# Kernel tuning notes

Hardware: AMD Instinct MI355X
Metric: run time of the kernel (lower is better)

## Reference

```python
import jax, jax.numpy as jnp
import numpy as np

E, IN, H1, H2, H3, A, B = 20, 512, 1024, 512, 256, 32, 4096


def setup_inputs() -> dict:
    key = jax.random.key(0)
    ks = jax.random.split(key, 10)

    def w(k, shape, fan_in):
        return jax.random.normal(k, shape, dtype=jnp.float32) / np.sqrt(fan_in)

    return {
        "obs": jax.random.normal(ks[0], (B, IN), dtype=jnp.float32),
        # stacked expert MLP params [E, ...]
        "eW1": w(ks[1], (E, IN, H1), IN), "eb1": jnp.zeros((E, H1), jnp.float32),
        "eW2": w(ks[2], (E, H1, H2), H1), "eb2": jnp.zeros((E, H2), jnp.float32),
        "eW3": w(ks[3], (E, H2, H3), H2), "eb3": jnp.zeros((E, H3), jnp.float32),
        "eW4": w(ks[4], (E, H3, A), H3), "eb4": jnp.zeros((E, A), jnp.float32),
        # gate MLP params
        "gW1": w(ks[5], (IN, H1), IN), "gb1": jnp.zeros((H1,), jnp.float32),
        "gW2": w(ks[6], (H1, H2), H1), "gb2": jnp.zeros((H2,), jnp.float32),
        "gW3": w(ks[7], (H2, H3), H2), "gb3": jnp.zeros((H3,), jnp.float32),
        "gW4": w(ks[8], (H3, E), H3), "gb4": jnp.zeros((E,), jnp.float32),
    }


def _experts(obs, eW1, eb1, eW2, eb2, eW3, eb3, eW4, eb4):
    # batched over experts: [B, E, h]
    h = jax.nn.elu(jnp.einsum('bi,eih->beh', obs, eW1) + eb1[None])
    h = jax.nn.elu(jnp.einsum('beh,ehk->bek', h, eW2) + eb2[None])
    h = jax.nn.elu(jnp.einsum('bek,ekm->bem', h, eW3) + eb3[None])
    return jnp.einsum('bem,ema->bea', h, eW4) + eb4[None]  # [B, E, A]


def _gate(obs, gW1, gb1, gW2, gb2, gW3, gb3, gW4, gb4):
    h = jax.nn.elu(obs @ gW1 + gb1)
    h = jax.nn.elu(h @ gW2 + gb2)
    h = jax.nn.elu(h @ gW3 + gb3)
    return jax.nn.softmax(h @ gW4 + gb4, axis=-1)  # [B, E]


def reference(obs, eW1, eb1, eW2, eb2, eW3, eb3, eW4, eb4,
              gW1, gb1, gW2, gb2, gW3, gb3, gW4, gb4):
    weights = _gate(obs, gW1, gb1, gW2, gb2, gW3, gb3, gW4, gb4)       # [B, E]
    actions = _experts(obs, eW1, eb1, eW2, eb2, eW3, eb3, eW4, eb4)    # [B, E, A]
    # bmm(weights[:,None,:], actions).squeeze(1)
    return jnp.einsum('be,bea->ba', weights, actions)                   # [B, A]
```

## Files before the change

kernel.cpp:

```cpp
#include <hip/hip_runtime.h>

#define B_SZ 4096
#define E_EXP 20
#define NE 21

typedef unsigned short u16;
typedef __bf16 bf16x8 __attribute__((ext_vector_type(8)));
typedef u16 u16x8 __attribute__((ext_vector_type(8)));
typedef u16 u16x4 __attribute__((ext_vector_type(4)));
typedef float floatx4 __attribute__((ext_vector_type(4)));

static __device__ __forceinline__ u16 f2bf(float f) {
  unsigned u = __builtin_bit_cast(unsigned, f);
  u += 0x7fffu + ((u >> 16) & 1u);
  return (u16)(u >> 16);
}

static __device__ __forceinline__ float elu1(float v) {
  return v > 0.f ? v : (__expf(v) - 1.f);
}

static __device__ __forceinline__ bf16x8 ld_bf8(const u16* p) {
  u16x8 v = *reinterpret_cast<const u16x8*>(p);
  return __builtin_bit_cast(bf16x8, v);
}

static __device__ __forceinline__ void gld_lds16(const u16* g, u16* l) {
  __builtin_amdgcn_global_load_lds(
      (const __attribute__((address_space(1))) unsigned int*)g,
      (__attribute__((address_space(3))) unsigned int*)l, 16, 0, 0);
}


__global__ void convert_obs_kernel(const float* __restrict__ src,
                                   u16* __restrict__ dst, int n) {
  int i = (blockIdx.x * blockDim.x + threadIdx.x) * 4;
  if (i < n) {
    float4 v = *reinterpret_cast<const float4*>(src + i);
    u16x4 o;
    o.x = f2bf(v.x); o.y = f2bf(v.y); o.z = f2bf(v.z); o.w = f2bf(v.w);
    *reinterpret_cast<u16x4*>(dst + i) = o;
  }
}

__global__ __launch_bounds__(256) void transpose_conv_kernel(
    const float* __restrict__ src_e, const float* __restrict__ src_g,
    int n_e, int K, int N, int Nout, u16* __restrict__ dst) {
  int e = blockIdx.z;
  const float* src = (e < n_e) ? (src_e + (long)e * K * N) : src_g;
  __shared__ float t[64][65];
  int tid = threadIdx.x;
  int kbase = blockIdx.x * 64;
  int nbase = blockIdx.y * 64;

  int kk = tid >> 4;
  int n4 = (tid & 15) * 4;
#pragma unroll
  for (int p = 0; p < 4; ++p) {
    int k = kbase + p * 16 + kk;
    int n = nbase + n4;
    float4 v = make_float4(0.f, 0.f, 0.f, 0.f);
    if (n + 3 < N) {
      v = *reinterpret_cast<const float4*>(&src[(long)k * N + n]);
    } else {
      float* vp = &v.x;
      for (int j = 0; j < 4; ++j)
        if (n + j < N) vp[j] = src[(long)k * N + n + j];
    }
    t[p * 16 + kk][n4 + 0] = v.x;
    t[p * 16 + kk][n4 + 1] = v.y;
    t[p * 16 + kk][n4 + 2] = v.z;
    t[p * 16 + kk][n4 + 3] = v.w;
  }
  __syncthreads();

  u16* dstE = dst + (long)e * Nout * K;
  int kk8 = (tid & 7) * 8;
#pragma unroll
  for (int p = 0; p < 2; ++p) {
    int ln = p * 32 + (tid >> 3);
    int n = nbase + ln;
    if (n < Nout) {
      u16x8 o;
#pragma unroll
      for (int j = 0; j < 8; ++j) o[j] = f2bf(t[kk8 + j][ln]);
      *reinterpret_cast<u16x8*>(&dstE[(long)n * K + kbase + kk8]) = o;
    }
  }
}

__global__ void concat_bias3_kernel(
    const float* __restrict__ eb1, const float* __restrict__ gb1,
    const float* __restrict__ eb2, const float* __restrict__ gb2,
    const float* __restrict__ eb3, const float* __restrict__ gb3,
    float* __restrict__ b1, float* __restrict__ b2, float* __restrict__ b3) {
  int i = blockIdx.x * blockDim.x + threadIdx.x;
  const int S1 = NE * 1024, S2 = NE * 512, S3 = NE * 256;
  if (i < S1) {
    b1[i] = (i < E_EXP * 1024) ? eb1[i] : gb1[i - E_EXP * 1024];
  } else if (i < S1 + S2) {
    int j = i - S1;
    b2[j] = (j < E_EXP * 512) ? eb2[j] : gb2[j - E_EXP * 512];
  } else if (i < S1 + S2 + S3) {
    int j = i - S1 - S2;
    b3[j] = (j < E_EXP * 256) ? eb3[j] : gb3[j - E_EXP * 256];
  }
}

#define BM 128
#define BN 128

__global__ __launch_bounds__(256) void gemm_bias_elu_kernel(
    const u16* __restrict__ A_base, long a_estride,
    const u16* __restrict__ Wt_base, long w_estride,
    const float* __restrict__ bias_base, long b_estride,
    u16* __restrict__ C_base, long c_estride,
    int M, int N, int K) {
  int e = blockIdx.z;
  const u16* A = A_base + (long)e * a_estride;
  const u16* Wt = Wt_base + (long)e * w_estride;
  const float* bias = bias_base + (long)e * b_estride;
  u16* C = C_base + (long)e * c_estride;

  int m0 = blockIdx.y * BM;
  int n0 = blockIdx.x * BN;

  __shared__ u16 As[2 * BM * 32];
  __shared__ u16 Bs[2 * BN * 32];

  int tid = threadIdx.x;
  int lane = tid & 63;
  int w = tid >> 6;
  int wm = (w >> 1) * 64;
  int wn = (w & 1) * 64;
  int col = lane & 15;
  int quad = lane >> 4;

  floatx4 acc[4][4] = {};

  int srow = tid >> 2;
  int scol = (tid & 3) * 8;
  const u16* gA0 = &A[(long)(m0 + srow) * K + scol];
  const u16* gA1 = gA0 + (long)64 * K;
  const u16* gB0 = &Wt[(long)(n0 + srow) * K + scol];
  const u16* gB1 = gB0 + (long)64 * K;

  for (int k0 = 0; k0 < K; k0 += 64) {
    __syncthreads();
    gld_lds16(gA0 + k0, &As[(size_t)tid * 8]);
    gld_lds16(gA1 + k0, &As[(size_t)(256 + tid) * 8]);
    gld_lds16(gA0 + k0 + 32, &As[(size_t)(512 + tid) * 8]);
    gld_lds16(gA1 + k0 + 32, &As[(size_t)(768 + tid) * 8]);
    gld_lds16(gB0 + k0, &Bs[(size_t)tid * 8]);
    gld_lds16(gB1 + k0, &Bs[(size_t)(256 + tid) * 8]);
    gld_lds16(gB0 + k0 + 32, &Bs[(size_t)(512 + tid) * 8]);
    gld_lds16(gB1 + k0 + 32, &Bs[(size_t)(768 + tid) * 8]);
    __syncthreads();

#pragma unroll
    for (int kk = 0; kk < 2; ++kk) {
      bf16x8 xf[4], wf[4];
#pragma unroll
      for (int t = 0; t < 4; ++t) {
        xf[t] = __builtin_bit_cast(bf16x8,
            *reinterpret_cast<u16x8*>(
                &As[kk * BM * 32 + (wm + t * 16 + col) * 32 + quad * 8]));
        wf[t] = __builtin_bit_cast(bf16x8,
            *reinterpret_cast<u16x8*>(
                &Bs[kk * BN * 32 + (wn + t * 16 + col) * 32 + quad * 8]));
      }
#pragma unroll
      for (int i = 0; i < 4; ++i)
#pragma unroll
        for (int j = 0; j < 4; ++j)
          acc[i][j] = __builtin_amdgcn_mfma_f32_16x16x32_bf16(
              wf[j], xf[i], acc[i][j], 0, 0, 0);
    }
  }

#pragma unroll
  for (int j = 0; j < 4; ++j) {
    int nn = n0 + wn + j * 16 + quad * 4;
    float4 b4 = *reinterpret_cast<const float4*>(&bias[nn]);
#pragma unroll
    for (int i = 0; i < 4; ++i) {
      int m = m0 + wm + i * 16 + col;
      u16x4 o;
      o.x = f2bf(elu1(acc[i][j][0] + b4.x));
      o.y = f2bf(elu1(acc[i][j][1] + b4.y));
      o.z = f2bf(elu1(acc[i][j][2] + b4.z));
      o.w = f2bf(elu1(acc[i][j][3] + b4.w));
      *reinterpret_cast<u16x4*>(&C[(long)m * N + nn]) = o;
    }
  }
}

__global__ __launch_bounds__(256) void final_combine_kernel(
    const u16* __restrict__ h3, const u16* __restrict__ W4t,
    const u16* __restrict__ gW4t, const float* __restrict__ eb4,
    const float* __restrict__ gb4, float* __restrict__ out) {
  const int H3 = 256;
  int tid = threadIdx.x;
  int lane = tid & 63;
  int w = tid >> 6;
  int col = lane & 15;
  int quad = lane >> 4;
  int r0 = blockIdx.x * 16;

  floatx4 g0 = {}, g1 = {};
  const u16* h3g = h3 + (long)E_EXP * B_SZ * H3;
#pragma unroll
  for (int k0 = 0; k0 < 256; k0 += 32) {
    bf16x8 a = ld_bf8(&h3g[(long)(r0 + col) * H3 + k0 + quad * 8]);
    bf16x8 b0 = ld_bf8(&gW4t[(long)col * H3 + k0 + quad * 8]);
    bf16x8 b1 = ld_bf8(&gW4t[(long)(16 + col) * H3 + k0 + quad * 8]);
    g0 = __builtin_amdgcn_mfma_f32_16x16x32_bf16(a, b0, g0, 0, 0, 0);
    g1 = __builtin_amdgcn_mfma_f32_16x16x32_bf16(a, b1, g1, 0, 0, 0);
  }

  float w0[4], w1[4];
  float gbc0 = gb4[col];
  float gbc1 = (col < 4) ? gb4[16 + col] : 0.f;
#pragma unroll
  for (int r = 0; r < 4; ++r) {
    float v0 = g0[r] + gbc0;
    float v1 = (col < 4) ? (g1[r] + gbc1) : -1e30f;
    float m = fmaxf(v0, v1);
#pragma unroll
    for (int s = 1; s < 16; s <<= 1) m = fmaxf(m, __shfl_xor(m, s, 64));
    float e0 = __expf(v0 - m);
    float e1 = (col < 4) ? __expf(v1 - m) : 0.f;
    float ssum = e0 + e1;
#pragma unroll
    for (int s = 1; s < 16; s <<= 1) ssum += __shfl_xor(ssum, s, 64);
    w0[r] = e0 / ssum;
    w1[r] = e1 / ssum;
  }

  floatx4 o0 = {}, o1 = {};
  for (int e = w; e < E_EXP; e += 4) {
    floatx4 a0 = {}, a1 = {};
    const u16* he = h3 + (long)e * B_SZ * H3;
    const u16* we = W4t + (long)e * 32 * H3;
#pragma unroll
    for (int k0 = 0; k0 < 256; k0 += 32) {
      bf16x8 a = ld_bf8(&he[(long)(r0 + col) * H3 + k0 + quad * 8]);
      bf16x8 b0 = ld_bf8(&we[(long)col * H3 + k0 + quad * 8]);
      bf16x8 b1 = ld_bf8(&we[(long)(16 + col) * H3 + k0 + quad * 8]);
      a0 = __builtin_amdgcn_mfma_f32_16x16x32_bf16(a, b0, a0, 0, 0, 0);
      a1 = __builtin_amdgcn_mfma_f32_16x16x32_bf16(a, b1, a1, 0, 0, 0);
    }
    float be0 = eb4[e * 32 + col];
    float be1 = eb4[e * 32 + 16 + col];
    int src = (lane & 48) + (e & 15);
#pragma unroll
    for (int r = 0; r < 4; ++r) {
      float wr = __shfl((e < 16) ? w0[r] : w1[r], src, 64);
      o0[r] += wr * (a0[r] + be0);
      o1[r] += wr * (a1[r] + be1);
    }
  }

  __shared__ float red[3][64][8];
  if (w > 0) {
#pragma unroll
    for (int r = 0; r < 4; ++r) {
      red[w - 1][lane][r] = o0[r];
      red[w - 1][lane][4 + r] = o1[r];
    }
  }
  __syncthreads();
  if (w == 0) {
#pragma unroll
    for (int ww = 0; ww < 3; ++ww)
#pragma unroll
      for (int r = 0; r < 4; ++r) {
        o0[r] += red[ww][lane][r];
        o1[r] += red[ww][lane][4 + r];
      }
#pragma unroll
    for (int r = 0; r < 4; ++r) {
      int row = r0 + quad * 4 + r;
      out[(long)row * 32 + col] = o0[r];
      out[(long)row * 32 + 16 + col] = o1[r];
    }
  }
}


static inline size_t align256(size_t x) { return (x + 255) & ~(size_t)255; }

extern "C" void kernel_launch(void* const* d_in, const int* in_sizes, int n_in,
                              void* d_out, int out_size, void* d_ws,
                              size_t ws_size, hipStream_t stream) {
  const float* obs = (const float*)d_in[0];
  const float* eW1 = (const float*)d_in[1];
  const float* eb1 = (const float*)d_in[2];
  const float* eW2 = (const float*)d_in[3];
  const float* eb2 = (const float*)d_in[4];
  const float* eW3 = (const float*)d_in[5];
  const float* eb3 = (const float*)d_in[6];
  const float* eW4 = (const float*)d_in[7];
  const float* eb4 = (const float*)d_in[8];
  const float* gW1 = (const float*)d_in[9];
  const float* gb1 = (const float*)d_in[10];
  const float* gW2 = (const float*)d_in[11];
  const float* gb2 = (const float*)d_in[12];
  const float* gW3 = (const float*)d_in[13];
  const float* gb3 = (const float*)d_in[14];
  const float* gW4 = (const float*)d_in[15];
  const float* gb4 = (const float*)d_in[16];
  float* out = (float*)d_out;
  char* ws = (char*)d_ws;

  size_t off = 0;
  size_t OFF_OBS = off;  off = align256(off + (size_t)B_SZ * 512 * 2);
  size_t OFF_W1T = off;  off = align256(off + (size_t)NE * 1024 * 512 * 2);
  size_t OFF_W2T = off;  off = align256(off + (size_t)NE * 512 * 1024 * 2);
  size_t OFF_W3T = off;  off = align256(off + (size_t)NE * 256 * 512 * 2);
  size_t OFF_W4T = off;  off = align256(off + (size_t)E_EXP * 32 * 256 * 2);
  size_t OFF_GW4T = off; off = align256(off + (size_t)32 * 256 * 2);
  size_t OFF_B1 = off;   off = align256(off + (size_t)NE * 1024 * 4);
  size_t OFF_B2 = off;   off = align256(off + (size_t)NE * 512 * 4);
  size_t OFF_B3 = off;   off = align256(off + (size_t)NE * 256 * 4);
  size_t OFF_H3 = off;   off = align256(off + (size_t)NE * B_SZ * 256 * 2);

  int chunk = B_SZ;
  size_t OFF_H1 = off;
  while (chunk > 512) {
    size_t need = (size_t)NE * chunk * 1024 * 2 + (size_t)NE * chunk * 512 * 2;
    if (OFF_H1 + need <= ws_size) break;
    chunk >>= 1;
  }
  size_t OFF_H2 = align256(OFF_H1 + (size_t)NE * chunk * 1024 * 2);

  u16* obs_bf = (u16*)(ws + OFF_OBS);
  u16* W1t = (u16*)(ws + OFF_W1T);
  u16* W2t = (u16*)(ws + OFF_W2T);
  u16* W3t = (u16*)(ws + OFF_W3T);
  u16* W4t = (u16*)(ws + OFF_W4T);
  u16* gW4t = (u16*)(ws + OFF_GW4T);
  float* b1 = (float*)(ws + OFF_B1);
  float* b2 = (float*)(ws + OFF_B2);
  float* b3 = (float*)(ws + OFF_B3);
  u16* h3 = (u16*)(ws + OFF_H3);
  u16* h1 = (u16*)(ws + OFF_H1);
  u16* h2 = (u16*)(ws + OFF_H2);

  convert_obs_kernel<<<(B_SZ * 512 / 4 + 255) / 256, 256, 0, stream>>>(
      obs, obs_bf, B_SZ * 512);
  transpose_conv_kernel<<<dim3(8, 16, NE), 256, 0, stream>>>(
      eW1, gW1, E_EXP, 512, 1024, 1024, W1t);
  transpose_conv_kernel<<<dim3(16, 8, NE), 256, 0, stream>>>(
      eW2, gW2, E_EXP, 1024, 512, 512, W2t);
  transpose_conv_kernel<<<dim3(8, 4, NE), 256, 0, stream>>>(
      eW3, gW3, E_EXP, 512, 256, 256, W3t);
  transpose_conv_kernel<<<dim3(4, 1, E_EXP), 256, 0, stream>>>(
      eW4, nullptr, E_EXP, 256, 32, 32, W4t);
  transpose_conv_kernel<<<dim3(4, 1, 1), 256, 0, stream>>>(
      gW4, nullptr, 1, 256, 20, 32, gW4t);
  concat_bias3_kernel<<<(NE * 1792 + 255) / 256, 256, 0, stream>>>(
      eb1, gb1, eb2, gb2, eb3, gb3, b1, b2, b3);

  for (int bc = 0; bc < B_SZ; bc += chunk) {
    gemm_bias_elu_kernel<<<dim3(1024 / BN, chunk / BM, NE), 256, 0, stream>>>(
        obs_bf + (size_t)bc * 512, 0L,
        W1t, (long)1024 * 512,
        b1, 1024L,
        h1, (long)chunk * 1024, chunk, 1024, 512);
    gemm_bias_elu_kernel<<<dim3(512 / BN, chunk / BM, NE), 256, 0, stream>>>(
        h1, (long)chunk * 1024,
        W2t, (long)512 * 1024,
        b2, 512L,
        h2, (long)chunk * 512, chunk, 512, 1024);
    gemm_bias_elu_kernel<<<dim3(256 / BN, chunk / BM, NE), 256, 0, stream>>>(
        h2, (long)chunk * 512,
        W3t, (long)256 * 512,
        b3, 256L,
        h3 + (size_t)bc * 256, (long)B_SZ * 256, chunk, 256, 512);
  }

  final_combine_kernel<<<B_SZ / 16, 256, 0, stream>>>(h3, W4t, gW4t, eb4, gb4,
                                                      out);
}
```

Before: 551.4 us.

## Merge prep kernels and enlarge GEMM M-tile to 256 rows

Folds the obs conversion and bias concatenation into one launch, and the five weight transpose launches into one flat-indexed kernel, which cuts launch overhead and tail gaps. The GEMM tile grows from 128x128 to 256x128, so each wave holds an 8x4 accumulator grid, raising MFMA work per LDS load. The launch bounds request two blocks per CU. The larger tile needs more registers and LDS and halves the number of blocks in the M dimension, which can hurt occupancy and load balance for small chunks.

```diff
diff --git a/kernel.cpp b/kernel.cpp
--- a/kernel.cpp
+++ b/kernel.cpp
@@ -32,27 +32,72 @@
 }
 
 
-__global__ void convert_obs_kernel(const float* __restrict__ src,
-                                   u16* __restrict__ dst, int n) {
-  int i = (blockIdx.x * blockDim.x + threadIdx.x) * 4;
-  if (i < n) {
-    float4 v = *reinterpret_cast<const float4*>(src + i);
+__global__ void prep_small_kernel(
+    const float* __restrict__ obs, u16* __restrict__ obs_bf,
+    const float* __restrict__ eb1, const float* __restrict__ gb1,
+    const float* __restrict__ eb2, const float* __restrict__ gb2,
+    const float* __restrict__ eb3, const float* __restrict__ gb3,
+    float* __restrict__ b1, float* __restrict__ b2, float* __restrict__ b3) {
+  int bid = blockIdx.x;
+  if (bid < 2048) {
+    int i = (bid * 256 + threadIdx.x) * 4;
+    float4 v = *reinterpret_cast<const float4*>(obs + i);
     u16x4 o;
     o.x = f2bf(v.x); o.y = f2bf(v.y); o.z = f2bf(v.z); o.w = f2bf(v.w);
-    *reinterpret_cast<u16x4*>(dst + i) = o;
-  }
-}
-
-__global__ __launch_bounds__(256) void transpose_conv_kernel(
-    const float* __restrict__ src_e, const float* __restrict__ src_g,
-    int n_e, int K, int N, int Nout, u16* __restrict__ dst) {
-  int e = blockIdx.z;
-  const float* src = (e < n_e) ? (src_e + (long)e * K * N) : src_g;
-  __shared__ float t[64][65];
+    *reinterpret_cast<u16x4*>(obs_bf + i) = o;
+  } else {
+    int i = (bid - 2048) * 256 + threadIdx.x;
+    const int S1 = NE * 1024, S2 = NE * 512, S3 = NE * 256;
+    if (i < S1) {
+      b1[i] = (i < E_EXP * 1024) ? eb1[i] : gb1[i - E_EXP * 1024];
+    } else if (i < S1 + S2) {
+      int j = i - S1;
+      b2[j] = (j < E_EXP * 512) ? eb2[j] : gb2[j - E_EXP * 512];
+    } else if (i < S1 + S2 + S3) {
+      int j = i - S1 - S2;
+      b3[j] = (j < E_EXP * 256) ? eb3[j] : gb3[j - E_EXP * 256];
+    }
+  }
+}
+
+#define TRANS_BLOCKS 6132
+
+__global__ __launch_bounds__(256) void transpose_all_kernel(
+    const float* __restrict__ eW1, const float* __restrict__ gW1,
+    const float* __restrict__ eW2, const float* __restrict__ gW2,
+    const float* __restrict__ eW3, const float* __restrict__ gW3,
+    const float* __restrict__ eW4, const float* __restrict__ gW4,
+    u16* __restrict__ W1t, u16* __restrict__ W2t, u16* __restrict__ W3t,
+    u16* __restrict__ W4t, u16* __restrict__ gW4t) {
+  int f = blockIdx.x;
+  const float *srcE, *srcG;
+  u16* dstBase;
+  int rem, K, N, Nout, kxt, tpm, nm;
+  if (f < 2688) {
+    rem = f;        srcE = eW1; srcG = gW1; dstBase = W1t;
+    K = 512;  N = 1024; Nout = 1024; kxt = 8;  tpm = 128; nm = 20;
+  } else if (f < 5376) {
+    rem = f - 2688; srcE = eW2; srcG = gW2; dstBase = W2t;
+    K = 1024; N = 512;  Nout = 512;  kxt = 16; tpm = 128; nm = 20;
+  } else if (f < 6048) {
+    rem = f - 5376; srcE = eW3; srcG = gW3; dstBase = W3t;
+    K = 512;  N = 256;  Nout = 256;  kxt = 8;  tpm = 32;  nm = 20;
+  } else if (f < 6128) {
+    rem = f - 6048; srcE = eW4; srcG = nullptr; dstBase = W4t;
+    K = 256;  N = 32;   Nout = 32;   kxt = 4;  tpm = 4;   nm = 99;
+  } else {
+    rem = f - 6128; srcE = gW4; srcG = nullptr; dstBase = gW4t;
+    K = 256;  N = 20;   Nout = 32;   kxt = 4;  tpm = 4;   nm = 99;
+  }
+  int mat = rem / tpm;
+  int t = rem % tpm;
+  const float* src = (mat < nm) ? (srcE + (long)mat * K * N) : srcG;
+  u16* dst = dstBase + (long)mat * Nout * K;
+  int kbase = (t % kxt) * 64;
+  int nbase = (t / kxt) * 64;
+
+  __shared__ float tl[64][65];
   int tid = threadIdx.x;
-  int kbase = blockIdx.x * 64;
-  int nbase = blockIdx.y * 64;
-
   int kk = tid >> 4;
   int n4 = (tid & 15) * 4;
 #pragma unroll
@@ -67,14 +112,13 @@
       for (int j = 0; j < 4; ++j)
         if (n + j < N) vp[j] = src[(long)k * N + n + j];
     }
-    t[p * 16 + kk][n4 + 0] = v.x;
-    t[p * 16 + kk][n4 + 1] = v.y;
-    t[p * 16 + kk][n4 + 2] = v.z;
-    t[p * 16 + kk][n4 + 3] = v.w;
+    tl[p * 16 + kk][n4 + 0] = v.x;
+    tl[p * 16 + kk][n4 + 1] = v.y;
+    tl[p * 16 + kk][n4 + 2] = v.z;
+    tl[p * 16 + kk][n4 + 3] = v.w;
   }
   __syncthreads();
 
-  u16* dstE = dst + (long)e * Nout * K;
   int kk8 = (tid & 7) * 8;
 #pragma unroll
   for (int p = 0; p < 2; ++p) {
@@ -83,34 +127,17 @@
     if (n < Nout) {
       u16x8 o;
 #pragma unroll
-      for (int j = 0; j < 8; ++j) o[j] = f2bf(t[kk8 + j][ln]);
-      *reinterpret_cast<u16x8*>(&dstE[(long)n * K + kbase + kk8]) = o;
-    }
-  }
-}
-
-__global__ void concat_bias3_kernel(
-    const float* __restrict__ eb1, const float* __restrict__ gb1,
-    const float* __restrict__ eb2, const float* __restrict__ gb2,
-    const float* __restrict__ eb3, const float* __restrict__ gb3,
-    float* __restrict__ b1, float* __restrict__ b2, float* __restrict__ b3) {
-  int i = blockIdx.x * blockDim.x + threadIdx.x;
-  const int S1 = NE * 1024, S2 = NE * 512, S3 = NE * 256;
-  if (i < S1) {
-    b1[i] = (i < E_EXP * 1024) ? eb1[i] : gb1[i - E_EXP * 1024];
-  } else if (i < S1 + S2) {
-    int j = i - S1;
-    b2[j] = (j < E_EXP * 512) ? eb2[j] : gb2[j - E_EXP * 512];
-  } else if (i < S1 + S2 + S3) {
-    int j = i - S1 - S2;
-    b3[j] = (j < E_EXP * 256) ? eb3[j] : gb3[j - E_EXP * 256];
-  }
-}
-
-#define BM 128
+      for (int j = 0; j < 8; ++j) o[j] = f2bf(tl[kk8 + j][ln]);
+      *reinterpret_cast<u16x8*>(&dst[(long)n * K + kbase + kk8]) = o;
+    }
+  }
+}
+
+
+#define BM 256
 #define BN 128
 
-__global__ __launch_bounds__(256) void gemm_bias_elu_kernel(
+__global__ __launch_bounds__(256, 2) void gemm_bias_elu_kernel(
     const u16* __restrict__ A_base, long a_estride,
     const u16* __restrict__ Wt_base, long w_estride,
     const float* __restrict__ bias_base, long b_estride,
@@ -131,46 +158,49 @@
   int tid = threadIdx.x;
   int lane = tid & 63;
   int w = tid >> 6;
-  int wm = (w >> 1) * 64;
+  int wm = (w >> 1) * 128;
   int wn = (w & 1) * 64;
   int col = lane & 15;
   int quad = lane >> 4;
 
-  floatx4 acc[4][4] = {};
+  floatx4 acc[8][4] = {};
 
   int srow = tid >> 2;
   int scol = (tid & 3) * 8;
-  const u16* gA0 = &A[(long)(m0 + srow) * K + scol];
-  const u16* gA1 = gA0 + (long)64 * K;
-  const u16* gB0 = &Wt[(long)(n0 + srow) * K + scol];
-  const u16* gB1 = gB0 + (long)64 * K;
+  const u16* gA = &A[(long)(m0 + srow) * K + scol];
+  const u16* gB = &Wt[(long)(n0 + srow) * K + scol];
 
   for (int k0 = 0; k0 < K; k0 += 64) {
     __syncthreads();
-    gld_lds16(gA0 + k0, &As[(size_t)tid * 8]);
-    gld_lds16(gA1 + k0, &As[(size_t)(256 + tid) * 8]);
-    gld_lds16(gA0 + k0 + 32, &As[(size_t)(512 + tid) * 8]);
-    gld_lds16(gA1 + k0 + 32, &As[(size_t)(768 + tid) * 8]);
-    gld_lds16(gB0 + k0, &Bs[(size_t)tid * 8]);
-    gld_lds16(gB1 + k0, &Bs[(size_t)(256 + tid) * 8]);
-    gld_lds16(gB0 + k0 + 32, &Bs[(size_t)(512 + tid) * 8]);
-    gld_lds16(gB1 + k0 + 32, &Bs[(size_t)(768 + tid) * 8]);
+    gld_lds16(gA + k0,                 &As[(size_t)tid * 8]);
+    gld_lds16(gA + (long)64 * K + k0,  &As[2048 + (size_t)tid * 8]);
+    gld_lds16(gA + (long)128 * K + k0, &As[4096 + (size_t)tid * 8]);
+    gld_lds16(gA + (long)192 * K + k0, &As[6144 + (size_t)tid * 8]);
+    gld_lds16(gA + k0 + 32,                 &As[8192 + (size_t)tid * 8]);
+    gld_lds16(gA + (long)64 * K + k0 + 32,  &As[10240 + (size_t)tid * 8]);
+    gld_lds16(gA + (long)128 * K + k0 + 32, &As[12288 + (size_t)tid * 8]);
+    gld_lds16(gA + (long)192 * K + k0 + 32, &As[14336 + (size_t)tid * 8]);
+    gld_lds16(gB + k0,                &Bs[(size_t)tid * 8]);
+    gld_lds16(gB + (long)64 * K + k0, &Bs[2048 + (size_t)tid * 8]);
+    gld_lds16(gB + k0 + 32,                &Bs[4096 + (size_t)tid * 8]);
+    gld_lds16(gB + (long)64 * K + k0 + 32, &Bs[6144 + (size_t)tid * 8]);
     __syncthreads();
 
 #pragma unroll
     for (int kk = 0; kk < 2; ++kk) {
-      bf16x8 xf[4], wf[4];
-#pragma unroll
-      for (int t = 0; t < 4; ++t) {
+      bf16x8 xf[8], wf[4];
+#pragma unroll
+      for (int t = 0; t < 8; ++t)
         xf[t] = __builtin_bit_cast(bf16x8,
             *reinterpret_cast<u16x8*>(
-                &As[kk * BM * 32 + (wm + t * 16 + col) * 32 + quad * 8]));
+                &As[kk * 8192 + (wm + t * 16 + col) * 32 + quad * 8]));
+#pragma unroll
+      for (int t = 0; t < 4; ++t)
         wf[t] = __builtin_bit_cast(bf16x8,
             *reinterpret_cast<u16x8*>(
-                &Bs[kk * BN * 32 + (wn + t * 16 + col) * 32 + quad * 8]));
-      }
-#pragma unroll
-      for (int i = 0; i < 4; ++i)
+                &Bs[kk * 4096 + (wn + t * 16 + col) * 32 + quad * 8]));
+#pragma unroll
+      for (int i = 0; i < 8; ++i)
 #pragma unroll
         for (int j = 0; j < 4; ++j)
           acc[i][j] = __builtin_amdgcn_mfma_f32_16x16x32_bf16(
@@ -183,7 +213,7 @@
     int nn = n0 + wn + j * 16 + quad * 4;
     float4 b4 = *reinterpret_cast<const float4*>(&bias[nn]);
 #pragma unroll
-    for (int i = 0; i < 4; ++i) {
+    for (int i = 0; i < 8; ++i) {
       int m = m0 + wm + i * 16 + col;
       u16x4 o;
       o.x = f2bf(elu1(acc[i][j][0] + b4.x));
@@ -347,20 +377,10 @@
   u16* h1 = (u16*)(ws + OFF_H1);
   u16* h2 = (u16*)(ws + OFF_H2);
 
-  convert_obs_kernel<<<(B_SZ * 512 / 4 + 255) / 256, 256, 0, stream>>>(
-      obs, obs_bf, B_SZ * 512);
-  transpose_conv_kernel<<<dim3(8, 16, NE), 256, 0, stream>>>(
-      eW1, gW1, E_EXP, 512, 1024, 1024, W1t);
-  transpose_conv_kernel<<<dim3(16, 8, NE), 256, 0, stream>>>(
-      eW2, gW2, E_EXP, 1024, 512, 512, W2t);
-  transpose_conv_kernel<<<dim3(8, 4, NE), 256, 0, stream>>>(
-      eW3, gW3, E_EXP, 512, 256, 256, W3t);
-  transpose_conv_kernel<<<dim3(4, 1, E_EXP), 256, 0, stream>>>(
-      eW4, nullptr, E_EXP, 256, 32, 32, W4t);
-  transpose_conv_kernel<<<dim3(4, 1, 1), 256, 0, stream>>>(
-      gW4, nullptr, 1, 256, 20, 32, gW4t);
-  concat_bias3_kernel<<<(NE * 1792 + 255) / 256, 256, 0, stream>>>(
-      eb1, gb1, eb2, gb2, eb3, gb3, b1, b2, b3);
+  prep_small_kernel<<<2048 + (NE * 1792 + 255) / 256, 256, 0, stream>>>(
+      obs, obs_bf, eb1, gb1, eb2, gb2, eb3, gb3, b1, b2, b3);
+  transpose_all_kernel<<<TRANS_BLOCKS, 256, 0, stream>>>(
+      eW1, gW1, eW2, gW2, eW3, gW3, eW4, gW4, W1t, W2t, W3t, W4t, gW4t);
 
   for (int bc = 0; bc < B_SZ; bc += chunk) {
     gemm_bias_elu_kernel<<<dim3(1024 / BN, chunk / BM, NE), 256, 0, stream>>>(
```

Measured after the change: 557.9 us. Within noise of the previous version (+1.2%).
